# Performance work log

Hardware: AMD Instinct MI355X
Metric: run time of the kernel (lower is better)

Reference implementation:

```python
import jax, jax.numpy as jnp
import numpy as np

B, N = 32, 512
IN, HID, HEADS, OUT = 128, 32, 4, 128
NEG_SLOPE = 0.2


def _ln(x, g, b, eps=1e-5):
    mu = x.mean(-1, keepdims=True)
    var = ((x - mu) ** 2).mean(-1, keepdims=True)
    return (x - mu) * jax.lax.rsqrt(var + eps) * g + b


def _gat(x, adj_mask, W, a_src, a_dst, average):
    # x: [B,N,F], adj_mask: [B,1,N,N] bool, W: [F,H,D], a_*: [H,D]
    h = jnp.einsum('bnf,fhd->bnhd', x, W)                      # [B,N,H,D]
    e_src = jnp.einsum('bnhd,hd->bhn', h, a_src)               # [B,H,N]
    e_dst = jnp.einsum('bnhd,hd->bhn', h, a_dst)
    e = jax.nn.leaky_relu(e_src[:, :, :, None] + e_dst[:, :, None, :], NEG_SLOPE)  # [B,H,N,N]
    e = jnp.where(adj_mask, e, jnp.asarray(-1e9, e.dtype))
    att = jax.nn.softmax(e, axis=-1)                           # masked softmax over neighbors
    out = jnp.einsum('bhnm,bmhd->bnhd', att, h)                # aggregate neighbor features
    if average:
        return out.mean(axis=2)                                # [B,N,D]
    return out.reshape(out.shape[0], out.shape[1], -1)         # concat heads [B,N,H*D]


def setup_inputs() -> dict:
    key = jax.random.key(0)
    ks = jax.random.split(key, 16)
    def nrm(k, shape, scale=0.05):
        return jax.random.normal(k, shape, dtype=jnp.float32) * scale
    return {
        'x': jax.random.normal(ks[0], (B, N, IN), dtype=jnp.float32),
        'graph': jax.random.randint(ks[1], (B, N, N), 0, 2, dtype=jnp.int32),
        'W0': nrm(ks[2], (IN, HEADS, HID)),
        'a_src0': nrm(ks[3], (HEADS, HID)),
        'a_dst0': nrm(ks[4], (HEADS, HID)),
        'W1': nrm(ks[5], (HEADS * HID, 1, OUT)),
        'a_src1': nrm(ks[6], (1, OUT)),
        'a_dst1': nrm(ks[7], (1, OUT)),
        'ln1_g': jnp.ones((IN + OUT,), jnp.float32), 'ln1_b': jnp.zeros((IN + OUT,), jnp.float32),
        'lin_W': nrm(ks[8], (IN + OUT, OUT)), 'lin_b': jnp.zeros((OUT,), jnp.float32),
        'me_W0': nrm(ks[9], (OUT, OUT)), 'me_b0': jnp.zeros((OUT,), jnp.float32),
        'me_W1': nrm(ks[10], (OUT, OUT)), 'me_b1': jnp.zeros((OUT,), jnp.float32),
        'ln2_g': jnp.ones((OUT,), jnp.float32), 'ln2_b': jnp.zeros((OUT,), jnp.float32),
        'oh_W': nrm(ks[11], (OUT, OUT)), 'oh_b': jnp.zeros((OUT,), jnp.float32),
        'ln3_g': jnp.ones((OUT,), jnp.float32), 'ln3_b': jnp.zeros((OUT,), jnp.float32),
    }


def reference(x, graph, W0, a_src0, a_dst0, W1, a_src1, a_dst1,
              ln1_g, ln1_b, lin_W, lin_b, me_W0, me_b0, me_W1, me_b1,
              ln2_g, ln2_b, oh_W, oh_b, ln3_g, ln3_b):
    eye = jnp.eye(N, dtype=bool)
    adj_mask = ((graph > 0) | eye)[:, None, :, :]              # self-loops, [B,1,N,N]
    m = _gat(x, adj_mask, W0, a_src0, a_dst0, average=False)   # [B,N,HEADS*HID]
    m = jax.nn.elu(m)
    m = _gat(m, adj_mask, W1, a_src1, a_dst1, average=True)    # [B,N,OUT]
    m = _ln(jnp.concatenate([x, m], axis=-1), ln1_g, ln1_b)    # ln1
    m = m @ lin_W + lin_b                                      # linear
    enc = jax.nn.gelu(m @ me_W0 + me_b0, approximate=False) @ me_W1 + me_b1
    out = _ln(m + enc, ln2_g, ln2_b)                           # ln2(residual)
    out = jax.nn.gelu(out @ oh_W + oh_b, approximate=False)
    out = _ln(out, ln3_g, ln3_b)                               # LN inside output_head
    return out
```

## Files before the change

### kernel.cpp

```cpp
#include <hip/hip_runtime.h>
#include <cmath>


typedef unsigned short ushort_t;
typedef __attribute__((ext_vector_type(8))) short short8;
typedef __attribute__((ext_vector_type(4))) float f32x4;

__device__ __forceinline__ float gelu_f(float v) {
    return 0.5f * v * (1.0f + erff(v * 0.70710678118654752f));
}
__device__ __forceinline__ ushort_t f2bf(float x) {
    union { float f; unsigned u; } v; v.f = x;
    return (ushort_t)((v.u + 0x7FFFu + ((v.u >> 16) & 1u)) >> 16);
}
__device__ __forceinline__ ushort_t f2bf_t(float x) {
    union { float f; unsigned u; } v; v.f = x;
    return (ushort_t)(v.u >> 16);
}

__device__ __forceinline__ void gload_lds16(const ushort_t* g, ushort_t* l) {
    __builtin_amdgcn_global_load_lds((__attribute__((address_space(1))) void*)g,
                                     (__attribute__((address_space(3))) void*)l, 16, 0, 0);
}
__device__ __forceinline__ void stage_chunk(const ushort_t* src, ushort_t* dst,
                                            int wv, int lane) {
#pragma unroll
    for (int i = 0; i < 4; i++) {
        int rbase = wv * 32 + i * 8;
        gload_lds16(src + (rbase + (lane >> 3)) * 512 + (lane & 7) * 8,
                    dst + rbase * 64);
    }
}

__global__ __launch_bounds__(256) void prep_wt(const float* __restrict__ lin_W,
        const float* __restrict__ me_W0, const float* __restrict__ me_W1,
        const float* __restrict__ oh_W, const float* __restrict__ W0,
        const float* __restrict__ W1, ushort_t* __restrict__ WT) {
    int i = blockIdx.x * 256 + threadIdx.x;
    if (i < 32768)       { int c = i >> 8, k = i & 255;                   WT[i] = f2bf(lin_W[k * 128 + c]); }
    else if (i < 49152)  { int j = i - 32768;  int c = j >> 7, k = j & 127; WT[i] = f2bf(me_W0[k * 128 + c]); }
    else if (i < 65536)  { int j = i - 49152;  int c = j >> 7, k = j & 127; WT[i] = f2bf(me_W1[k * 128 + c]); }
    else if (i < 81920)  { int j = i - 65536;  int c = j >> 7, k = j & 127; WT[i] = f2bf(oh_W[k * 128 + c]); }
    else if (i < 98304)  { int j = i - 81920;  int c = j >> 7, k = j & 127; WT[i] = f2bf(W0[k * 128 + c]); }
    else if (i < 114688) { int j = i - 98304;  int c = j >> 7, k = j & 127; WT[i] = f2bf(W1[k * 128 + c]); }
}

__global__ __launch_bounds__(256) void pack_graph(const int* __restrict__ g,
                                                  unsigned* __restrict__ gm) {
    int idx = blockIdx.x * 256 + threadIdx.x;
    const int4* gp = (const int4*)g + (size_t)idx * 8;
    unsigned m = 0;
#pragma unroll
    for (int q = 0; q < 8; q++) {
        int4 v = gp[q];
        m |= (unsigned)(v.x > 0) << (q * 4 + 0);
        m |= (unsigned)(v.y > 0) << (q * 4 + 1);
        m |= (unsigned)(v.z > 0) << (q * 4 + 2);
        m |= (unsigned)(v.w > 0) << (q * 4 + 3);
    }
    gm[idx] = m;
}

__global__ __launch_bounds__(256) void gemm_mfma0(const float* __restrict__ X,
        const ushort_t* __restrict__ WTr, ushort_t* __restrict__ Ht,
        const float* __restrict__ a_s, const float* __restrict__ a_d,
        float* __restrict__ es, float* __restrict__ ed) {
    __shared__ __align__(16) ushort_t abuf[16 * 128];
    __shared__ __align__(16) ushort_t tb[128 * 24];
    __shared__ float2 ered[8 * 16];
    const int tid = threadIdx.x;
    const int row0 = blockIdx.x * 16;
    const int b = row0 >> 9, m0 = row0 & 511;
    const int w = tid >> 6, lane = tid & 63;
    const int quad = lane >> 4, lid = lane & 15;
    {
        int r = tid >> 4, g = tid & 15;
        const float4* src = (const float4*)(X + (row0 + r) * 128 + g * 8);
        float4 a = src[0], bb = src[1];
        short8 p;
        p[0] = (short)f2bf(a.x);  p[1] = (short)f2bf(a.y);
        p[2] = (short)f2bf(a.z);  p[3] = (short)f2bf(a.w);
        p[4] = (short)f2bf(bb.x); p[5] = (short)f2bf(bb.y);
        p[6] = (short)f2bf(bb.z); p[7] = (short)f2bf(bb.w);
        *(short8*)&abuf[r * 128 + ((g ^ (r & 7)) * 8)] = p;
    }
    __syncthreads();
    short8 af[4];
#pragma unroll
    for (int kc = 0; kc < 4; kc++)
        af[kc] = *(const short8*)&abuf[lid * 128 + (((kc * 4 + quad) ^ (lid & 7)) * 8)];
    f32x4 C[2];
#pragma unroll
    for (int i = 0; i < 2; i++) {
        int ct = w + 4 * i;
        const ushort_t* bp = WTr + (ct * 16 + lid) * 128 + quad * 8;
        C[i] = (f32x4){0.f, 0.f, 0.f, 0.f};
#pragma unroll
        for (int kc = 0; kc < 4; kc++) {
            short8 bf = *(const short8*)&bp[kc * 32];
            C[i] = __builtin_amdgcn_mfma_f32_16x16x32_bf16(af[kc], bf, C[i], 0, 0, 0);
        }
    }
#pragma unroll
    for (int i = 0; i < 2; i++) {
        int ct = w + 4 * i, col = ct * 16 + lid;
        float as_c = a_s[col], ad_c = a_d[col];
        float s0[4], d0[4];
#pragma unroll
        for (int r = 0; r < 4; r++) { s0[r] = C[i][r] * as_c; d0[r] = C[i][r] * ad_c; }
#pragma unroll
        for (int st = 1; st <= 8; st <<= 1)
#pragma unroll
            for (int r = 0; r < 4; r++) {
                s0[r] += __shfl_xor(s0[r], st);
                d0[r] += __shfl_xor(d0[r], st);
            }
        if (lid == 0) {
#pragma unroll
            for (int r = 0; r < 4; r++)
                ered[ct * 16 + quad * 4 + r] = make_float2(s0[r], d0[r]);
        }
#pragma unroll
        for (int r = 0; r < 4; r++)
            tb[col * 24 + quad * 4 + r] = f2bf(C[i][r]);
    }
    __syncthreads();
    if (tid < 64) {
        int row = tid & 15, h = tid >> 4;
        float2 pa = ered[(2 * h) * 16 + row], pb = ered[(2 * h + 1) * 16 + row];
        es[(b * 4 + h) * 512 + m0 + row] = pa.x + pb.x;
        ed[(b * 4 + h) * 512 + m0 + row] = pa.y + pb.y;
    }
    {
        int c = tid >> 1, half = tid & 1;
        int m = m0 + half * 8;
        int msw = (m & ~63) | ((((m >> 3) ^ c) & 7) << 3);
        *(short8*)&Ht[b * 65536 + c * 512 + msw] = *(const short8*)&tb[c * 24 + half * 8];
    }
}

__global__ __launch_bounds__(256) void gat0_gemm(const ushort_t* __restrict__ Ht0,
        const float* __restrict__ es0, const float* __restrict__ ed0,
        const unsigned* __restrict__ gmask, const ushort_t* __restrict__ W1T,
        const float* __restrict__ a_s, const float* __restrict__ a_d,
        ushort_t* __restrict__ Ht1, float* __restrict__ es1, float* __restrict__ ed1) {
    __shared__ __align__(16) char smem[40960];
    ushort_t* hsb0 = (ushort_t*)smem;
    ushort_t* hsb1 = (ushort_t*)(smem + 16384);
    float*    eds  = (float*)(smem + 32768);
    ushort_t* abuf = (ushort_t*)(smem + 32768);
    ushort_t* tb   = (ushort_t*)smem;
    float2*   ered = (float2*)(smem + 6144);
    const int tid = threadIdx.x;
    const int b = blockIdx.y, n0 = blockIdx.x * 16;
    const int wv = tid >> 6, lane = tid & 63;
    const int quad = lane >> 4, lid = lane & 15;
    const int n = n0 + lid;
    const ushort_t* hsrc = Ht0 + b * 65536;
    const float es_v = es0[b * 2048 + wv * 512 + n];
    const unsigned* gmrow = gmask + (b * 512 + n) * 16;
    uint4 gq0 = *(const uint4*)(gmrow);
    uint4 gq1 = *(const uint4*)(gmrow + 4);
    uint4 gq2 = *(const uint4*)(gmrow + 8);
    uint4 gq3 = *(const uint4*)(gmrow + 12);
    const unsigned mw[16] = {gq0.x, gq0.y, gq0.z, gq0.w, gq1.x, gq1.y, gq1.z, gq1.w,
                             gq2.x, gq2.y, gq2.z, gq2.w, gq3.x, gq3.y, gq3.z, gq3.w};
    {
        const float4* src = (const float4*)(ed0 + b * 2048);
        float4 v0 = src[tid * 2], v1 = src[tid * 2 + 1];
        ((float4*)eds)[tid * 2] = v0;
        ((float4*)eds)[tid * 2 + 1] = v1;
    }
    __builtin_amdgcn_sched_barrier(0);
    stage_chunk(hsrc, hsb0, wv, lane);
    __builtin_amdgcn_sched_barrier(0);
    asm volatile("s_waitcnt lgkmcnt(0)" ::: "memory");
    __builtin_amdgcn_s_barrier();
    __builtin_amdgcn_sched_barrier(0);
    const short8 onesf = {0x3F80, 0x3F80, 0x3F80, 0x3F80, 0x3F80, 0x3F80, 0x3F80, 0x3F80};
    f32x4 acc[2], dsf;
    acc[0] = (f32x4){0.f, 0.f, 0.f, 0.f};
    acc[1] = (f32x4){0.f, 0.f, 0.f, 0.f};
    dsf = (f32x4){0.f, 0.f, 0.f, 0.f};
#pragma unroll
    for (int t = 0; t < 8; t++) {
        ushort_t* cbuf = (t & 1) ? hsb1 : hsb0;
        short8 af[2];
#pragma unroll
        for (int kc = 0; kc < 2; kc++) {
            const int base = t * 64 + kc * 32 + quad * 8;
            unsigned mb8 = (mw[2 * t + kc] >> (quad * 8)) & 0xffu;
            if ((unsigned)(n - base) < 8u) mb8 |= 1u << (n - base);
            float4 e0v = *(const float4*)&eds[wv * 512 + base];
            float4 e1v = *(const float4*)&eds[wv * 512 + base + 4];
            float ev[8] = {e0v.x, e0v.y, e0v.z, e0v.w, e1v.x, e1v.y, e1v.z, e1v.w};
            short8 pk;
#pragma unroll
            for (int j = 0; j < 8; j++) {
                float e = es_v + ev[j];
                e = fmaxf(e, 0.2f * e);
                e = ((mb8 >> j) & 1u) ? e : -1e30f;
                pk[j] = (short)f2bf_t(__expf(e));
            }
            af[kc] = pk;
        }
        if (t < 7) stage_chunk(hsrc + (t + 1) * 64, (t & 1) ? hsb0 : hsb1, wv, lane);
        __builtin_amdgcn_sched_barrier(0);
        if (t < 7) asm volatile("s_waitcnt vmcnt(4)" ::: "memory");
        else       asm volatile("s_waitcnt vmcnt(0)" ::: "memory");
        __builtin_amdgcn_sched_barrier(0);
#pragma unroll
        for (int kc = 0; kc < 2; kc++) {
            const int gsw = ((kc * 4 + quad) ^ (lid & 7)) * 8;
            short8 b0 = *(const short8*)&cbuf[(wv * 32 + lid) * 64 + gsw];
            short8 b1 = *(const short8*)&cbuf[(wv * 32 + 16 + lid) * 64 + gsw];
            acc[0] = __builtin_amdgcn_mfma_f32_16x16x32_bf16(af[kc], b0, acc[0], 0, 0, 0);
            acc[1] = __builtin_amdgcn_mfma_f32_16x16x32_bf16(af[kc], b1, acc[1], 0, 0, 0);
            dsf = __builtin_amdgcn_mfma_f32_16x16x32_bf16(af[kc], onesf, dsf, 0, 0, 0);
        }
    }
    __syncthreads();
#pragma unroll
    for (int reg = 0; reg < 4; reg++) {
        float inv = 1.0f / dsf[reg];
        int rw = quad * 4 + reg;
#pragma unroll
        for (int ch = 0; ch < 2; ch++) {
            float v = acc[ch][reg] * inv;
            v = v > 0.f ? v : expm1f(v);
            int col = wv * 32 + ch * 16 + lid;
            abuf[rw * 128 + (((col >> 3) ^ (rw & 7)) * 8) + (col & 7)] = f2bf(v);
        }
    }
    __syncthreads();
    short8 af[4];
#pragma unroll
    for (int kc = 0; kc < 4; kc++)
        af[kc] = *(const short8*)&abuf[lid * 128 + (((kc * 4 + quad) ^ (lid & 7)) * 8)];
    f32x4 C[2];
#pragma unroll
    for (int i = 0; i < 2; i++) {
        int ct = wv + 4 * i;
        const ushort_t* bp = W1T + (ct * 16 + lid) * 128 + quad * 8;
        C[i] = (f32x4){0.f, 0.f, 0.f, 0.f};
#pragma unroll
        for (int kc = 0; kc < 4; kc++) {
            short8 bf = *(const short8*)&bp[kc * 32];
            C[i] = __builtin_amdgcn_mfma_f32_16x16x32_bf16(af[kc], bf, C[i], 0, 0, 0);
        }
    }
#pragma unroll
    for (int i = 0; i < 2; i++) {
        int ct = wv + 4 * i, col = ct * 16 + lid;
        float as_c = a_s[col], ad_c = a_d[col];
        float s0[4], d0[4];
#pragma unroll
        for (int r = 0; r < 4; r++) { s0[r] = C[i][r] * as_c; d0[r] = C[i][r] * ad_c; }
#pragma unroll
        for (int st = 1; st <= 8; st <<= 1)
#pragma unroll
            for (int r = 0; r < 4; r++) {
                s0[r] += __shfl_xor(s0[r], st);
                d0[r] += __shfl_xor(d0[r], st);
            }
        if (lid == 0) {
#pragma unroll
            for (int r = 0; r < 4; r++)
                ered[ct * 16 + quad * 4 + r] = make_float2(s0[r], d0[r]);
        }
#pragma unroll
        for (int r = 0; r < 4; r++)
            tb[col * 24 + quad * 4 + r] = f2bf(C[i][r]);
    }
    __syncthreads();
    if (tid < 16) {
        float S = 0.f, D = 0.f;
#pragma unroll
        for (int ct = 0; ct < 8; ct++) { float2 p = ered[ct * 16 + tid]; S += p.x; D += p.y; }
        es1[b * 512 + n0 + tid] = S;
        ed1[b * 512 + n0 + tid] = D;
    }
    {
        int c = tid >> 1, half = tid & 1;
        int m = n0 + half * 8;
        int msw = (m & ~63) | ((((m >> 3) ^ c) & 7) << 3);
        *(short8*)&Ht1[b * 65536 + c * 512 + msw] = *(const short8*)&tb[c * 24 + half * 8];
    }
}

__global__ __launch_bounds__(256) void gat1_head(const ushort_t* __restrict__ Ht,
        const float* __restrict__ es1, const float* __restrict__ ed1,
        const unsigned* __restrict__ gmask, const float* __restrict__ x,
        const float* __restrict__ g1, const float* __restrict__ b1,
        const ushort_t* __restrict__ linT, const float* __restrict__ LB,
        const ushort_t* __restrict__ meT0, const float* __restrict__ B0,
        const ushort_t* __restrict__ meT1, const float* __restrict__ B1,
        const float* __restrict__ g2, const float* __restrict__ b2,
        const ushort_t* __restrict__ ohT, const float* __restrict__ ob,
        const float* __restrict__ g3, const float* __restrict__ b3,
        float* __restrict__ out) {
    __shared__ __align__(16) char smem[34816];
    ushort_t* hsb0 = (ushort_t*)smem;
    ushort_t* hsb1 = (ushort_t*)(smem + 16384);
    float*    eds  = (float*)(smem + 32768);
    ushort_t* ybuf = (ushort_t*)smem;
    ushort_t* abuf = (ushort_t*)(smem + 8192);
    ushort_t* tbuf = (ushort_t*)(smem + 12288);
    float*    gbuf = (float*)(smem + 16384);
    float2*   red  = (float2*)(smem + 24832);
    float2*   mvs  = (float2*)(smem + 25344);
    const int tid = threadIdx.x;
    const int b = blockIdx.y, n0 = blockIdx.x * 16;
    const int wv = tid >> 6, lane = tid & 63;
    const int quad = lane >> 4, lid = lane & 15;
    const int n = n0 + lid;
    const ushort_t* hsrc = Ht + b * 65536;
    const float es_v = es1[b * 512 + n];
    const unsigned* gmrow = gmask + (b * 512 + n) * 16;
    uint4 gq0 = *(const uint4*)(gmrow);
    uint4 gq1 = *(const uint4*)(gmrow + 4);
    uint4 gq2 = *(const uint4*)(gmrow + 8);
    uint4 gq3 = *(const uint4*)(gmrow + 12);
    const unsigned mw[16] = {gq0.x, gq0.y, gq0.z, gq0.w, gq1.x, gq1.y, gq1.z, gq1.w,
                             gq2.x, gq2.y, gq2.z, gq2.w, gq3.x, gq3.y, gq3.z, gq3.w};
    {
        float2 edv = ((const float2*)(ed1 + b * 512))[tid];
        ((float2*)eds)[tid] = edv;
    }
    __builtin_amdgcn_sched_barrier(0);
    stage_chunk(hsrc, hsb0, wv, lane);
    __builtin_amdgcn_sched_barrier(0);
    asm volatile("s_waitcnt lgkmcnt(0)" ::: "memory");
    __builtin_amdgcn_s_barrier();
    __builtin_amdgcn_sched_barrier(0);
    const short8 onesf = {0x3F80, 0x3F80, 0x3F80, 0x3F80, 0x3F80, 0x3F80, 0x3F80, 0x3F80};
    f32x4 acc[2], dsf;
    acc[0] = (f32x4){0.f, 0.f, 0.f, 0.f};
    acc[1] = (f32x4){0.f, 0.f, 0.f, 0.f};
    dsf = (f32x4){0.f, 0.f, 0.f, 0.f};
#pragma unroll
    for (int t = 0; t < 8; t++) {
        ushort_t* cbuf = (t & 1) ? hsb1 : hsb0;
        short8 af[2];
#pragma unroll
        for (int kc = 0; kc < 2; kc++) {
            const int base = t * 64 + kc * 32 + quad * 8;
            unsigned mb8 = (mw[2 * t + kc] >> (quad * 8)) & 0xffu;
            if ((unsigned)(n - base) < 8u) mb8 |= 1u << (n - base);
            float4 e0v = *(const float4*)&eds[base];
            float4 e1v = *(const float4*)&eds[base + 4];
            float ev[8] = {e0v.x, e0v.y, e0v.z, e0v.w, e1v.x, e1v.y, e1v.z, e1v.w};
            short8 pk;
#pragma unroll
            for (int j = 0; j < 8; j++) {
                float e = es_v + ev[j];
                e = fmaxf(e, 0.2f * e);
                e = ((mb8 >> j) & 1u) ? e : -1e30f;
                pk[j] = (short)f2bf_t(__expf(e));
            }
            af[kc] = pk;
        }
        if (t < 7) stage_chunk(hsrc + (t + 1) * 64, (t & 1) ? hsb0 : hsb1, wv, lane);
        __builtin_amdgcn_sched_barrier(0);
        if (t < 7) asm volatile("s_waitcnt vmcnt(4)" ::: "memory");
        else       asm volatile("s_waitcnt vmcnt(0)" ::: "memory");
        __builtin_amdgcn_sched_barrier(0);
#pragma unroll
        for (int kc = 0; kc < 2; kc++) {
            const int gsw = ((kc * 4 + quad) ^ (lid & 7)) * 8;
            short8 b0 = *(const short8*)&cbuf[(wv * 32 + lid) * 64 + gsw];
            short8 b1 = *(const short8*)&cbuf[(wv * 32 + 16 + lid) * 64 + gsw];
            acc[0] = __builtin_amdgcn_mfma_f32_16x16x32_bf16(af[kc], b0, acc[0], 0, 0, 0);
            acc[1] = __builtin_amdgcn_mfma_f32_16x16x32_bf16(af[kc], b1, acc[1], 0, 0, 0);
            dsf = __builtin_amdgcn_mfma_f32_16x16x32_bf16(af[kc], onesf, dsf, 0, 0, 0);
        }
    }
    __syncthreads();
#pragma unroll
    for (int reg = 0; reg < 4; reg++) {
        float inv = 1.0f / dsf[reg];
        int rw = quad * 4 + reg;
#pragma unroll
        for (int ch = 0; ch < 2; ch++)
            gbuf[rw * 132 + wv * 32 + ch * 16 + lid] = acc[ch][reg] * inv;
    }
    __syncthreads();
    const int r = tid >> 4, c16 = tid & 15;
    const float4* xp = (const float4*)(x + (b * 512 + n0 + r) * 128);
    float4 vv4[4];
    float s = 0.f, ss = 0.f;
#pragma unroll
    for (int i = 0; i < 4; i++) {
        int c4 = c16 * 4 + i;
        float4 v = (c4 < 32) ? xp[c4] : *(const float4*)&gbuf[r * 132 + (c4 - 32) * 4];
        vv4[i] = v;
        s += v.x + v.y + v.z + v.w;
        ss += v.x * v.x + v.y * v.y + v.z * v.z + v.w * v.w;
    }
#pragma unroll
    for (int st = 1; st <= 8; st <<= 1) { s += __shfl_xor(s, st); ss += __shfl_xor(ss, st); }
    if (c16 == 0) {
        float mu = s * (1.f / 256.f);
        float var = ss * (1.f / 256.f) - mu * mu;
        mvs[r] = make_float2(mu, rsqrtf(var + 1e-5f));
    }
    __syncthreads();
    {
        float mu = mvs[r].x, rstd = mvs[r].y;
#pragma unroll
        for (int half = 0; half < 2; half++) {
            int g = c16 * 2 + half, c0 = g * 8;
            float va[8] = {vv4[half * 2].x, vv4[half * 2].y, vv4[half * 2].z, vv4[half * 2].w,
                           vv4[half * 2 + 1].x, vv4[half * 2 + 1].y, vv4[half * 2 + 1].z, vv4[half * 2 + 1].w};
            short8 p;
#pragma unroll
            for (int e = 0; e < 8; e++)
                p[e] = (short)f2bf((va[e] - mu) * rstd * g1[c0 + e] + b1[c0 + e]);
            *(short8*)&ybuf[r * 256 + ((g ^ (r & 7)) * 8)] = p;
        }
    }
    __syncthreads();
    short8 af8[8];
#pragma unroll
    for (int ks = 0; ks < 8; ks++)
        af8[ks] = *(const short8*)&ybuf[lid * 256 + (((ks * 4 + quad) ^ (lid & 7)) * 8)];
    f32x4 M2[2];
#pragma unroll
    for (int i = 0; i < 2; i++) {
        int ct = wv + 4 * i;
        const ushort_t* bp = linT + (ct * 16 + lid) * 256 + quad * 8;
        M2[i] = (f32x4){0.f, 0.f, 0.f, 0.f};
#pragma unroll
        for (int ks = 0; ks < 8; ks++) {
            short8 bf = *(const short8*)&bp[ks * 32];
            M2[i] = __builtin_amdgcn_mfma_f32_16x16x32_bf16(af8[ks], bf, M2[i], 0, 0, 0);
        }
        float bias = LB[ct * 16 + lid];
#pragma unroll
        for (int reg = 0; reg < 4; reg++) M2[i][reg] += bias;
        int col = ct * 16 + lid, g = col >> 3, pos = col & 7;
#pragma unroll
        for (int reg = 0; reg < 4; reg++) {
            int rw = quad * 4 + reg;
            abuf[rw * 128 + ((g ^ (rw & 7)) * 8) + pos] = f2bf(M2[i][reg]);
        }
    }
    __syncthreads();
    short8 at[4];
#pragma unroll
    for (int kc = 0; kc < 4; kc++)
        at[kc] = *(const short8*)&abuf[lid * 128 + (((kc * 4 + quad) ^ (lid & 7)) * 8)];
#pragma unroll
    for (int i = 0; i < 2; i++) {
        int ct = wv + 4 * i;
        const ushort_t* bp = meT0 + (ct * 16 + lid) * 128 + quad * 8;
        f32x4 C = (f32x4){0.f, 0.f, 0.f, 0.f};
#pragma unroll
        for (int kc = 0; kc < 4; kc++) {
            short8 bf = *(const short8*)&bp[kc * 32];
            C = __builtin_amdgcn_mfma_f32_16x16x32_bf16(at[kc], bf, C, 0, 0, 0);
        }
        int col = ct * 16 + lid, g = col >> 3, pos = col & 7;
        float bias = B0[col];
#pragma unroll
        for (int reg = 0; reg < 4; reg++) {
            int rw = quad * 4 + reg;
            tbuf[rw * 128 + ((g ^ (rw & 7)) * 8) + pos] = f2bf(gelu_f(C[reg] + bias));
        }
    }
    __syncthreads();
#pragma unroll
    for (int kc = 0; kc < 4; kc++)
        at[kc] = *(const short8*)&tbuf[lid * 128 + (((kc * 4 + quad) ^ (lid & 7)) * 8)];
    f32x4 R[2];
    float sr[4] = {0.f, 0.f, 0.f, 0.f}, ssr[4] = {0.f, 0.f, 0.f, 0.f};
#pragma unroll
    for (int i = 0; i < 2; i++) {
        int ct = wv + 4 * i;
        const ushort_t* bp = meT1 + (ct * 16 + lid) * 128 + quad * 8;
        f32x4 C = (f32x4){0.f, 0.f, 0.f, 0.f};
#pragma unroll
        for (int kc = 0; kc < 4; kc++) {
            short8 bf = *(const short8*)&bp[kc * 32];
            C = __builtin_amdgcn_mfma_f32_16x16x32_bf16(at[kc], bf, C, 0, 0, 0);
        }
        float bias = B1[ct * 16 + lid];
#pragma unroll
        for (int reg = 0; reg < 4; reg++) {
            float v = M2[i][reg] + C[reg] + bias;
            R[i][reg] = v;
            sr[reg] += v; ssr[reg] += v * v;
        }
    }
#pragma unroll
    for (int st = 1; st <= 8; st <<= 1)
#pragma unroll
        for (int reg = 0; reg < 4; reg++) {
            sr[reg] += __shfl_xor(sr[reg], st);
            ssr[reg] += __shfl_xor(ssr[reg], st);
        }
    if (lid == 0) {
#pragma unroll
        for (int reg = 0; reg < 4; reg++)
            red[wv * 16 + quad * 4 + reg] = make_float2(sr[reg], ssr[reg]);
    }
    __syncthreads();
    float mu2[4], rstd2[4];
#pragma unroll
    for (int reg = 0; reg < 4; reg++) {
        float S = 0.f, SS = 0.f;
#pragma unroll
        for (int w4 = 0; w4 < 4; w4++) {
            float2 p = red[w4 * 16 + quad * 4 + reg];
            S += p.x; SS += p.y;
        }
        mu2[reg] = S * (1.f / 128.f);
        float var = SS * (1.f / 128.f) - mu2[reg] * mu2[reg];
        rstd2[reg] = rsqrtf(var + 1e-5f);
    }
#pragma unroll
    for (int i = 0; i < 2; i++) {
        int col = (wv + 4 * i) * 16 + lid, g = col >> 3, pos = col & 7;
        float gv = g2[col], bv = b2[col];
#pragma unroll
        for (int reg = 0; reg < 4; reg++) {
            int rw = quad * 4 + reg;
            float v = (R[i][reg] - mu2[reg]) * rstd2[reg] * gv + bv;
            tbuf[rw * 128 + ((g ^ (rw & 7)) * 8) + pos] = f2bf(v);
        }
    }
    __syncthreads();
#pragma unroll
    for (int kc = 0; kc < 4; kc++)
        at[kc] = *(const short8*)&tbuf[lid * 128 + (((kc * 4 + quad) ^ (lid & 7)) * 8)];
    f32x4 V[2];
#pragma unroll
    for (int reg = 0; reg < 4; reg++) { sr[reg] = 0.f; ssr[reg] = 0.f; }
#pragma unroll
    for (int i = 0; i < 2; i++) {
        int ct = wv + 4 * i;
        const ushort_t* bp = ohT + (ct * 16 + lid) * 128 + quad * 8;
        f32x4 C = (f32x4){0.f, 0.f, 0.f, 0.f};
#pragma unroll
        for (int kc = 0; kc < 4; kc++) {
            short8 bf = *(const short8*)&bp[kc * 32];
            C = __builtin_amdgcn_mfma_f32_16x16x32_bf16(at[kc], bf, C, 0, 0, 0);
        }
        float bias = ob[ct * 16 + lid];
#pragma unroll
        for (int reg = 0; reg < 4; reg++) {
            float v = gelu_f(C[reg] + bias);
            V[i][reg] = v;
            sr[reg] += v; ssr[reg] += v * v;
        }
    }
#pragma unroll
    for (int st = 1; st <= 8; st <<= 1)
#pragma unroll
        for (int reg = 0; reg < 4; reg++) {
            sr[reg] += __shfl_xor(sr[reg], st);
            ssr[reg] += __shfl_xor(ssr[reg], st);
        }
    if (lid == 0) {
#pragma unroll
        for (int reg = 0; reg < 4; reg++)
            red[wv * 16 + quad * 4 + reg] = make_float2(sr[reg], ssr[reg]);
    }
    __syncthreads();
#pragma unroll
    for (int reg = 0; reg < 4; reg++) {
        float S = 0.f, SS = 0.f;
#pragma unroll
        for (int w4 = 0; w4 < 4; w4++) {
            float2 p = red[w4 * 16 + quad * 4 + reg];
            S += p.x; SS += p.y;
        }
        mu2[reg] = S * (1.f / 128.f);
        float var = SS * (1.f / 128.f) - mu2[reg] * mu2[reg];
        rstd2[reg] = rsqrtf(var + 1e-5f);
    }
#pragma unroll
    for (int i = 0; i < 2; i++) {
        int col = (wv + 4 * i) * 16 + lid;
        float gv = g3[col], bv = b3[col];
#pragma unroll
        for (int reg = 0; reg < 4; reg++)
            out[(b * 512 + n0 + quad * 4 + reg) * 128 + col] =
                (V[i][reg] - mu2[reg]) * rstd2[reg] * gv + bv;
    }
}

extern "C" void kernel_launch(void* const* d_in, const int* in_sizes, int n_in,
                              void* d_out, int out_size, void* d_ws, size_t ws_size,
                              hipStream_t stream) {
    const float* x      = (const float*)d_in[0];
    const int*   graph  = (const int*)d_in[1];
    const float* a_src0 = (const float*)d_in[3];
    const float* a_dst0 = (const float*)d_in[4];
    const float* a_src1 = (const float*)d_in[6];
    const float* a_dst1 = (const float*)d_in[7];
    float* out = (float*)d_out;

    float* ws  = (float*)d_ws;
    ushort_t* Ht0  = (ushort_t*)ws;
    ushort_t* Ht1  = Ht0 + 2097152;
    float*    e0s  = ws + 2097152;
    float*    e0d  = e0s + 65536;
    float*    e1s  = e0d + 65536;
    float*    e1d  = e1s + 16384;
    ushort_t* WT   = (ushort_t*)(e1d + 16384);
    ushort_t* linT = WT;
    ushort_t* meT0 = WT + 32768;
    ushort_t* meT1 = WT + 49152;
    ushort_t* ohT  = WT + 65536;
    ushort_t* W0T  = WT + 81920;
    ushort_t* W1T  = WT + 98304;
    unsigned* gmask = (unsigned*)(WT + 114688);

    prep_wt<<<448, 256, 0, stream>>>((const float*)d_in[10], (const float*)d_in[12],
                                     (const float*)d_in[14], (const float*)d_in[18],
                                     (const float*)d_in[2], (const float*)d_in[5], WT);
    pack_graph<<<1024, 256, 0, stream>>>(graph, gmask);
    gemm_mfma0<<<1024, 256, 0, stream>>>(x, W0T, Ht0, a_src0, a_dst0, e0s, e0d);
    gat0_gemm<<<dim3(32, 32), 256, 0, stream>>>(Ht0, e0s, e0d, gmask, W1T,
                                                a_src1, a_dst1, Ht1, e1s, e1d);
    gat1_head<<<dim3(32, 32), 256, 0, stream>>>(Ht1, e1s, e1d, gmask, x,
                                                (const float*)d_in[8], (const float*)d_in[9],
                                                linT, (const float*)d_in[11],
                                                meT0, (const float*)d_in[13],
                                                meT1, (const float*)d_in[15],
                                                (const float*)d_in[16], (const float*)d_in[17],
                                                ohT, (const float*)d_in[19],
                                                (const float*)d_in[20], (const float*)d_in[21],
                                                out);
}
```

Baseline: 185.4 us.

## Share attention-probability computation across waves via LDS in GAT layer-2 head kernel

Before this change, every one of the four waves computed the full 16x64 block of exp(leaky-relu) attention weights for each chunk, so that work was done four times over. Now each thread computes 4 entries, the block writes the 16x64 probability tile once into a swizzled LDS buffer, and all waves read their MFMA A operands from it. This cuts the redundant exp and mask work to a quarter. In exchange it adds LDS traffic and two block barriers per chunk iteration, which may hurt the overlap between loads and MFMA.

```diff
diff --git a/kernel.cpp b/kernel.cpp
--- a/kernel.cpp
+++ b/kernel.cpp
@@ -4,6 +4,7 @@
 
 typedef unsigned short ushort_t;
 typedef __attribute__((ext_vector_type(8))) short short8;
+typedef __attribute__((ext_vector_type(4))) short s16x4;
 typedef __attribute__((ext_vector_type(4))) float f32x4;
 
 __device__ __forceinline__ float gelu_f(float v) {
@@ -299,10 +300,11 @@
         const ushort_t* __restrict__ ohT, const float* __restrict__ ob,
         const float* __restrict__ g3, const float* __restrict__ b3,
         float* __restrict__ out) {
-    __shared__ __align__(16) char smem[34816];
+    __shared__ __align__(16) char smem[36864];
     ushort_t* hsb0 = (ushort_t*)smem;
     ushort_t* hsb1 = (ushort_t*)(smem + 16384);
-    float*    eds  = (float*)(smem + 32768);
+    ushort_t* ps   = (ushort_t*)(smem + 32768);
+    float*    eds  = (float*)(smem + 34816);
     ushort_t* ybuf = (ushort_t*)smem;
     ushort_t* abuf = (ushort_t*)(smem + 8192);
     ushort_t* tbuf = (ushort_t*)(smem + 12288);
@@ -313,23 +315,17 @@
     const int b = blockIdx.y, n0 = blockIdx.x * 16;
     const int wv = tid >> 6, lane = tid & 63;
     const int quad = lane >> 4, lid = lane & 15;
-    const int n = n0 + lid;
+    const int pn = tid >> 4, q = tid & 15, off = q * 4;
+    const int ng = n0 + pn;
     const ushort_t* hsrc = Ht + b * 65536;
-    const float es_v = es1[b * 512 + n];
-    const unsigned* gmrow = gmask + (b * 512 + n) * 16;
-    uint4 gq0 = *(const uint4*)(gmrow);
-    uint4 gq1 = *(const uint4*)(gmrow + 4);
-    uint4 gq2 = *(const uint4*)(gmrow + 8);
-    uint4 gq3 = *(const uint4*)(gmrow + 12);
-    const unsigned mw[16] = {gq0.x, gq0.y, gq0.z, gq0.w, gq1.x, gq1.y, gq1.z, gq1.w,
-                             gq2.x, gq2.y, gq2.z, gq2.w, gq3.x, gq3.y, gq3.z, gq3.w};
-    {
-        float2 edv = ((const float2*)(ed1 + b * 512))[tid];
-        ((float2*)eds)[tid] = edv;
-    }
-    __builtin_amdgcn_sched_barrier(0);
+    const float es_v = es1[b * 512 + ng];
+    const unsigned* gmrow = gmask + (b * 512 + ng) * 16;
+    unsigned mword[8];
+#pragma unroll
+    for (int t = 0; t < 8; t++) mword[t] = gmrow[2 * t + (q >> 3)];
+    float2 edv = ((const float2*)(ed1 + b * 512))[tid];
     stage_chunk(hsrc, hsb0, wv, lane);
-    __builtin_amdgcn_sched_barrier(0);
+    ((float2*)eds)[tid] = edv;
     asm volatile("s_waitcnt lgkmcnt(0)" ::: "memory");
     __builtin_amdgcn_s_barrier();
     __builtin_amdgcn_sched_barrier(0);
@@ -340,42 +336,42 @@
     dsf = (f32x4){0.f, 0.f, 0.f, 0.f};
 #pragma unroll
     for (int t = 0; t < 8; t++) {
+        const int mc = t * 64;
         ushort_t* cbuf = (t & 1) ? hsb1 : hsb0;
-        short8 af[2];
-#pragma unroll
-        for (int kc = 0; kc < 2; kc++) {
-            const int base = t * 64 + kc * 32 + quad * 8;
-            unsigned mb8 = (mw[2 * t + kc] >> (quad * 8)) & 0xffu;
-            if ((unsigned)(n - base) < 8u) mb8 |= 1u << (n - base);
-            float4 e0v = *(const float4*)&eds[base];
-            float4 e1v = *(const float4*)&eds[base + 4];
-            float ev[8] = {e0v.x, e0v.y, e0v.z, e0v.w, e1v.x, e1v.y, e1v.z, e1v.w};
-            short8 pk;
-#pragma unroll
-            for (int j = 0; j < 8; j++) {
-                float e = es_v + ev[j];
-                e = fmaxf(e, 0.2f * e);
-                e = ((mb8 >> j) & 1u) ? e : -1e30f;
-                pk[j] = (short)f2bf_t(__expf(e));
-            }
-            af[kc] = pk;
-        }
-        if (t < 7) stage_chunk(hsrc + (t + 1) * 64, (t & 1) ? hsb0 : hsb1, wv, lane);
-        __builtin_amdgcn_sched_barrier(0);
+        const int mbase = mc + off;
+        float4 ev4 = *(const float4*)&eds[mbase];
+        if (t < 7) stage_chunk(hsrc + mc + 64, (t & 1) ? hsb0 : hsb1, wv, lane);
+        unsigned mb4 = (mword[t] >> ((q & 7) * 4)) & 0xFu;
+        if ((unsigned)(ng - mbase) < 4u) mb4 |= 1u << (ng - mbase);
+        float ev[4] = {ev4.x, ev4.y, ev4.z, ev4.w};
+        s16x4 pk;
+#pragma unroll
+        for (int j = 0; j < 4; j++) {
+            float e = es_v + ev[j];
+            e = fmaxf(e, 0.2f * e);
+            e = ((mb4 >> j) & 1u) ? e : -1e30f;
+            pk[j] = (short)f2bf_t(__expf(e));
+        }
+        *(s16x4*)&ps[pn * 64 + (((off >> 3) ^ (pn & 7)) * 8) + (off & 7)] = pk;
         if (t < 7) asm volatile("s_waitcnt vmcnt(4)" ::: "memory");
         else       asm volatile("s_waitcnt vmcnt(0)" ::: "memory");
+        asm volatile("s_waitcnt lgkmcnt(0)" ::: "memory");
+        __builtin_amdgcn_s_barrier();
         __builtin_amdgcn_sched_barrier(0);
 #pragma unroll
         for (int kc = 0; kc < 2; kc++) {
             const int gsw = ((kc * 4 + quad) ^ (lid & 7)) * 8;
+            short8 a = *(const short8*)&ps[lid * 64 + gsw];
             short8 b0 = *(const short8*)&cbuf[(wv * 32 + lid) * 64 + gsw];
             short8 b1 = *(const short8*)&cbuf[(wv * 32 + 16 + lid) * 64 + gsw];
-            acc[0] = __builtin_amdgcn_mfma_f32_16x16x32_bf16(af[kc], b0, acc[0], 0, 0, 0);
-            acc[1] = __builtin_amdgcn_mfma_f32_16x16x32_bf16(af[kc], b1, acc[1], 0, 0, 0);
-            dsf = __builtin_amdgcn_mfma_f32_16x16x32_bf16(af[kc], onesf, dsf, 0, 0, 0);
-        }
-    }
-    __syncthreads();
+            acc[0] = __builtin_amdgcn_mfma_f32_16x16x32_bf16(a, b0, acc[0], 0, 0, 0);
+            acc[1] = __builtin_amdgcn_mfma_f32_16x16x32_bf16(a, b1, acc[1], 0, 0, 0);
+            dsf = __builtin_amdgcn_mfma_f32_16x16x32_bf16(a, onesf, dsf, 0, 0, 0);
+        }
+        __builtin_amdgcn_sched_barrier(0);
+        __builtin_amdgcn_s_barrier();
+        __builtin_amdgcn_sched_barrier(0);
+    }
 #pragma unroll
     for (int reg = 0; reg < 4; reg++) {
         float inv = 1.0f / dsf[reg];
```

New measurement: 184.5 us. About the same (-0.5%).

## Load H operand directly from global instead of LDS double-buffered staging

Applied to the files above, without the earlier changes.

Removes the async global-to-LDS double-buffered staging of the transposed feature matrix in both GAT aggregation kernels. Each lane now reads its B-operand fragments straight from global memory (L2-resident), and the XOR swizzle on the Ht writes is dropped to match. LDS use shrinks sharply, which may raise occupancy and removes the waitcnt/barrier pipelining. In exchange every wave issues its own uncached-in-LDS global loads, and load latency is no longer hidden by explicit prefetch.

```diff
diff --git a/kernel.cpp b/kernel.cpp
--- a/kernel.cpp
+++ b/kernel.cpp
@@ -16,20 +16,6 @@
 __device__ __forceinline__ ushort_t f2bf_t(float x) {
     union { float f; unsigned u; } v; v.f = x;
     return (ushort_t)(v.u >> 16);
-}
-
-__device__ __forceinline__ void gload_lds16(const ushort_t* g, ushort_t* l) {
-    __builtin_amdgcn_global_load_lds((__attribute__((address_space(1))) void*)g,
-                                     (__attribute__((address_space(3))) void*)l, 16, 0, 0);
-}
-__device__ __forceinline__ void stage_chunk(const ushort_t* src, ushort_t* dst,
-                                            int wv, int lane) {
-#pragma unroll
-    for (int i = 0; i < 4; i++) {
-        int rbase = wv * 32 + i * 8;
-        gload_lds16(src + (rbase + (lane >> 3)) * 512 + (lane & 7) * 8,
-                    dst + rbase * 64);
-    }
 }
 
 __global__ __launch_bounds__(256) void prep_wt(const float* __restrict__ lin_W,
@@ -133,9 +119,7 @@
     }
     {
         int c = tid >> 1, half = tid & 1;
-        int m = m0 + half * 8;
-        int msw = (m & ~63) | ((((m >> 3) ^ c) & 7) << 3);
-        *(short8*)&Ht[b * 65536 + c * 512 + msw] = *(const short8*)&tb[c * 24 + half * 8];
+        *(short8*)&Ht[b * 65536 + c * 512 + m0 + half * 8] = *(const short8*)&tb[c * 24 + half * 8];
     }
 }
 
@@ -144,19 +128,18 @@
         const unsigned* __restrict__ gmask, const ushort_t* __restrict__ W1T,
         const float* __restrict__ a_s, const float* __restrict__ a_d,
         ushort_t* __restrict__ Ht1, float* __restrict__ es1, float* __restrict__ ed1) {
-    __shared__ __align__(16) char smem[40960];
-    ushort_t* hsb0 = (ushort_t*)smem;
-    ushort_t* hsb1 = (ushort_t*)(smem + 16384);
-    float*    eds  = (float*)(smem + 32768);
-    ushort_t* abuf = (ushort_t*)(smem + 32768);
-    ushort_t* tb   = (ushort_t*)smem;
-    float2*   ered = (float2*)(smem + 6144);
+    __shared__ __align__(16) char smem[11264];
+    float*    eds  = (float*)smem;
+    ushort_t* abuf = (ushort_t*)smem;
+    ushort_t* tb   = (ushort_t*)(smem + 4096);
+    float2*   ered = (float2*)(smem + 10240);
     const int tid = threadIdx.x;
     const int b = blockIdx.y, n0 = blockIdx.x * 16;
     const int wv = tid >> 6, lane = tid & 63;
     const int quad = lane >> 4, lid = lane & 15;
     const int n = n0 + lid;
-    const ushort_t* hsrc = Ht0 + b * 65536;
+    const ushort_t* hp0 = Ht0 + b * 65536 + (wv * 32 + lid) * 512;
+    const ushort_t* hp1 = hp0 + 16 * 512;
     const float es_v = es0[b * 2048 + wv * 512 + n];
     const unsigned* gmrow = gmask + (b * 512 + n) * 16;
     uint4 gq0 = *(const uint4*)(gmrow);
@@ -171,12 +154,7 @@
         ((float4*)eds)[tid * 2] = v0;
         ((float4*)eds)[tid * 2 + 1] = v1;
     }
-    __builtin_amdgcn_sched_barrier(0);
-    stage_chunk(hsrc, hsb0, wv, lane);
-    __builtin_amdgcn_sched_barrier(0);
-    asm volatile("s_waitcnt lgkmcnt(0)" ::: "memory");
-    __builtin_amdgcn_s_barrier();
-    __builtin_amdgcn_sched_barrier(0);
+    __syncthreads();
     const short8 onesf = {0x3F80, 0x3F80, 0x3F80, 0x3F80, 0x3F80, 0x3F80, 0x3F80, 0x3F80};
     f32x4 acc[2], dsf;
     acc[0] = (f32x4){0.f, 0.f, 0.f, 0.f};
@@ -184,15 +162,15 @@
     dsf = (f32x4){0.f, 0.f, 0.f, 0.f};
 #pragma unroll
     for (int t = 0; t < 8; t++) {
-        ushort_t* cbuf = (t & 1) ? hsb1 : hsb0;
-        short8 af[2];
 #pragma unroll
         for (int kc = 0; kc < 2; kc++) {
-            const int base = t * 64 + kc * 32 + quad * 8;
+            const int moff = t * 64 + (kc * 4 + quad) * 8;
+            short8 b0 = *(const short8*)&hp0[moff];
+            short8 b1 = *(const short8*)&hp1[moff];
             unsigned mb8 = (mw[2 * t + kc] >> (quad * 8)) & 0xffu;
-            if ((unsigned)(n - base) < 8u) mb8 |= 1u << (n - base);
-            float4 e0v = *(const float4*)&eds[wv * 512 + base];
-            float4 e1v = *(const float4*)&eds[wv * 512 + base + 4];
+            if ((unsigned)(n - moff) < 8u) mb8 |= 1u << (n - moff);
+            float4 e0v = *(const float4*)&eds[wv * 512 + moff];
+            float4 e1v = *(const float4*)&eds[wv * 512 + moff + 4];
             float ev[8] = {e0v.x, e0v.y, e0v.z, e0v.w, e1v.x, e1v.y, e1v.z, e1v.w};
             short8 pk;
 #pragma unroll
@@ -202,21 +180,9 @@
                 e = ((mb8 >> j) & 1u) ? e : -1e30f;
                 pk[j] = (short)f2bf_t(__expf(e));
             }
-            af[kc] = pk;
-        }
-        if (t < 7) stage_chunk(hsrc + (t + 1) * 64, (t & 1) ? hsb0 : hsb1, wv, lane);
-        __builtin_amdgcn_sched_barrier(0);
-        if (t < 7) asm volatile("s_waitcnt vmcnt(4)" ::: "memory");
-        else       asm volatile("s_waitcnt vmcnt(0)" ::: "memory");
-        __builtin_amdgcn_sched_barrier(0);
-#pragma unroll
-        for (int kc = 0; kc < 2; kc++) {
-            const int gsw = ((kc * 4 + quad) ^ (lid & 7)) * 8;
-            short8 b0 = *(const short8*)&cbuf[(wv * 32 + lid) * 64 + gsw];
-            short8 b1 = *(const short8*)&cbuf[(wv * 32 + 16 + lid) * 64 + gsw];
-            acc[0] = __builtin_amdgcn_mfma_f32_16x16x32_bf16(af[kc], b0, acc[0], 0, 0, 0);
-            acc[1] = __builtin_amdgcn_mfma_f32_16x16x32_bf16(af[kc], b1, acc[1], 0, 0, 0);
-            dsf = __builtin_amdgcn_mfma_f32_16x16x32_bf16(af[kc], onesf, dsf, 0, 0, 0);
+            acc[0] = __builtin_amdgcn_mfma_f32_16x16x32_bf16(pk, b0, acc[0], 0, 0, 0);
+            acc[1] = __builtin_amdgcn_mfma_f32_16x16x32_bf16(pk, b1, acc[1], 0, 0, 0);
+            dsf = __builtin_amdgcn_mfma_f32_16x16x32_bf16(pk, onesf, dsf, 0, 0, 0);
         }
     }
     __syncthreads();
@@ -282,9 +248,7 @@
     }
     {
         int c = tid >> 1, half = tid & 1;
-        int m = n0 + half * 8;
-        int msw = (m & ~63) | ((((m >> 3) ^ c) & 7) << 3);
-        *(short8*)&Ht1[b * 65536 + c * 512 + msw] = *(const short8*)&tb[c * 24 + half * 8];
+        *(short8*)&Ht1[b * 65536 + c * 512 + n0 + half * 8] = *(const short8*)&tb[c * 24 + half * 8];
     }
 }
 
@@ -299,10 +263,8 @@
         const ushort_t* __restrict__ ohT, const float* __restrict__ ob,
         const float* __restrict__ g3, const float* __restrict__ b3,
         float* __restrict__ out) {
-    __shared__ __align__(16) char smem[34816];
-    ushort_t* hsb0 = (ushort_t*)smem;
-    ushort_t* hsb1 = (ushort_t*)(smem + 16384);
-    float*    eds  = (float*)(smem + 32768);
+    __shared__ __align__(16) char smem[25472];
+    float*    eds  = (float*)smem;
     ushort_t* ybuf = (ushort_t*)smem;
     ushort_t* abuf = (ushort_t*)(smem + 8192);
     ushort_t* tbuf = (ushort_t*)(smem + 12288);
@@ -314,7 +276,8 @@
     const int wv = tid >> 6, lane = tid & 63;
     const int quad = lane >> 4, lid = lane & 15;
     const int n = n0 + lid;
-    const ushort_t* hsrc = Ht + b * 65536;
+    const ushort_t* hp0 = Ht + b * 65536 + (wv * 32 + lid) * 512;
+    const ushort_t* hp1 = hp0 + 16 * 512;
     const float es_v = es1[b * 512 + n];
     const unsigned* gmrow = gmask + (b * 512 + n) * 16;
     uint4 gq0 = *(const uint4*)(gmrow);
@@ -327,12 +290,7 @@
         float2 edv = ((const float2*)(ed1 + b * 512))[tid];
         ((float2*)eds)[tid] = edv;
     }
-    __builtin_amdgcn_sched_barrier(0);
-    stage_chunk(hsrc, hsb0, wv, lane);
-    __builtin_amdgcn_sched_barrier(0);
-    asm volatile("s_waitcnt lgkmcnt(0)" ::: "memory");
-    __builtin_amdgcn_s_barrier();
-    __builtin_amdgcn_sched_barrier(0);
+    __syncthreads();
     const short8 onesf = {0x3F80, 0x3F80, 0x3F80, 0x3F80, 0x3F80, 0x3F80, 0x3F80, 0x3F80};
     f32x4 acc[2], dsf;
     acc[0] = (f32x4){0.f, 0.f, 0.f, 0.f};
@@ -340,15 +298,15 @@
     dsf = (f32x4){0.f, 0.f, 0.f, 0.f};
 #pragma unroll
     for (int t = 0; t < 8; t++) {
-        ushort_t* cbuf = (t & 1) ? hsb1 : hsb0;
-        short8 af[2];
 #pragma unroll
         for (int kc = 0; kc < 2; kc++) {
-            const int base = t * 64 + kc * 32 + quad * 8;
+            const int moff = t * 64 + (kc * 4 + quad) * 8;
+            short8 b0 = *(const short8*)&hp0[moff];
+            short8 b1 = *(const short8*)&hp1[moff];
             unsigned mb8 = (mw[2 * t + kc] >> (quad * 8)) & 0xffu;
-            if ((unsigned)(n - base) < 8u) mb8 |= 1u << (n - base);
-            float4 e0v = *(const float4*)&eds[base];
-            float4 e1v = *(const float4*)&eds[base + 4];
+            if ((unsigned)(n - moff) < 8u) mb8 |= 1u << (n - moff);
+            float4 e0v = *(const float4*)&eds[moff];
+            float4 e1v = *(const float4*)&eds[moff + 4];
             float ev[8] = {e0v.x, e0v.y, e0v.z, e0v.w, e1v.x, e1v.y, e1v.z, e1v.w};
             short8 pk;
 #pragma unroll
@@ -358,21 +316,9 @@
                 e = ((mb8 >> j) & 1u) ? e : -1e30f;
                 pk[j] = (short)f2bf_t(__expf(e));
             }
-            af[kc] = pk;
-        }
-        if (t < 7) stage_chunk(hsrc + (t + 1) * 64, (t & 1) ? hsb0 : hsb1, wv, lane);
-        __builtin_amdgcn_sched_barrier(0);
-        if (t < 7) asm volatile("s_waitcnt vmcnt(4)" ::: "memory");
-        else       asm volatile("s_waitcnt vmcnt(0)" ::: "memory");
-        __builtin_amdgcn_sched_barrier(0);
-#pragma unroll
-        for (int kc = 0; kc < 2; kc++) {
-            const int gsw = ((kc * 4 + quad) ^ (lid & 7)) * 8;
-            short8 b0 = *(const short8*)&cbuf[(wv * 32 + lid) * 64 + gsw];
-            short8 b1 = *(const short8*)&cbuf[(wv * 32 + 16 + lid) * 64 + gsw];
-            acc[0] = __builtin_amdgcn_mfma_f32_16x16x32_bf16(af[kc], b0, acc[0], 0, 0, 0);
-            acc[1] = __builtin_amdgcn_mfma_f32_16x16x32_bf16(af[kc], b1, acc[1], 0, 0, 0);
-            dsf = __builtin_amdgcn_mfma_f32_16x16x32_bf16(af[kc], onesf, dsf, 0, 0, 0);
+            acc[0] = __builtin_amdgcn_mfma_f32_16x16x32_bf16(pk, b0, acc[0], 0, 0, 0);
+            acc[1] = __builtin_amdgcn_mfma_f32_16x16x32_bf16(pk, b1, acc[1], 0, 0, 0);
+            dsf = __builtin_amdgcn_mfma_f32_16x16x32_bf16(pk, onesf, dsf, 0, 0, 0);
         }
     }
     __syncthreads();
```

Result: slower. 194.4 us (+4.9%).
